# Kernel tuning notes

Hardware: AMD Instinct MI355X
Metric: run time of the kernel (lower is better)

Reference implementation:

```python
import jax, jax.numpy as jnp
import numpy as np

B, T, C = 256, 2048, 64  # batch, max_seq_len, num_classes


def setup_inputs() -> dict:
    key = jax.random.key(0)
    k1, k2, k3, k4 = jax.random.split(key, 4)
    pad_x = jax.random.normal(k1, (B, T, C), dtype=jnp.float32)
    transitions = jax.random.uniform(k2, (C, C), dtype=jnp.float32)
    origination = jax.random.uniform(k3, (C,), dtype=jnp.float32)
    batch_sizes = jnp.sort(jax.random.randint(k4, (B,), 1, T + 1))
    # the torch implementation assumes features are zero-padded past the length
    mask = jnp.arange(T)[None, :] < batch_sizes[:, None]  # (B, T)
    pad_x = pad_x * mask[:, :, None]
    return {"pad_x": pad_x, "transitions": transitions,
            "origination": origination, "batch_sizes": batch_sizes}


def reference(pad_x, transitions, origination, batch_sizes):
    # Linear-chain CRF forward algorithm (faithful to torch _forward_algo,
    # including the final sum over classes rather than logsumexp).
    x_tbc = jnp.swapaxes(pad_x, 0, 1)  # (T, B, C)
    alpha0 = x_tbc[0] + origination[None, :]  # (B, C)

    def step(alpha_prev, x_t):
        # scores[b, j, k] = alpha_prev[b, k] + transitions[j, k]
        scores = alpha_prev[:, None, :] + transitions[None, :, :]  # (B, C, C)
        alpha = x_t + jax.nn.logsumexp(scores, axis=2)  # (B, C)
        return alpha, alpha

    _, alphas_rest = jax.lax.scan(step, alpha0, x_tbc[1:])
    alphas = jnp.concatenate([alpha0[None], alphas_rest], axis=0)  # (T, B, C)
    # gather alpha at the last valid timestep of each sequence
    final = alphas[batch_sizes - 1, jnp.arange(pad_x.shape[0])]  # (B, C)
    return final.sum(axis=1)  # (B,)
```

## Files before the change

### kernel.cpp

```cpp
#include <hip/hip_runtime.h>


#define CC 64

typedef short bf16x8 __attribute__((ext_vector_type(8)));
typedef float f32x4 __attribute__((ext_vector_type(4)));

union PackAB { int w[4]; bf16x8 v; };

__device__ __forceinline__ int cvtpk(float lo, float hi) {
    int r;
    asm("v_cvt_pk_bf16_f32 %0, %1, %2" : "=v"(r) : "v"(lo), "v"(hi));
    return r;
}
__device__ __forceinline__ float bcast0(float v) {
    return __int_as_float(__builtin_amdgcn_readfirstlane(__float_as_int(v)));
}

#define LDS_FENCE() asm volatile("s_waitcnt lgkmcnt(0)" ::: "memory")

__launch_bounds__(64, 2)
__global__ void crf_seg_kernel(const float* __restrict__ x,
                               const float* __restrict__ trans,
                               const int*   __restrict__ lens,
                               unsigned short* __restrict__ Mws,
                               float* __restrict__ Ls,
                               int T, int Pseg, int Pshift, int SEG) {
    const int blk = blockIdx.x;
    const int b = blk >> Pshift;
    const int s = blk & (Pseg - 1);
    const int L = lens[b];
    const int tbeg = s * SEG;
    int segend = (s + 1) * SEG; if (segend > L - 1) segend = L - 1;
    const int nsteps = segend - tbeg;
    if (nsteps <= 0) return;

    const int l = threadIdx.x;
    const int c = l & 15, g = l >> 4;
    const float L2E = 1.4426950408889634f;
    const float* xb = x + (size_t)b * T * CC;

    __shared__ float xl[32][CC];

    {
        const int rl = l >> 4;
        const int cl = (l & 15) * 4;
        f32x4 st[8];
        #pragma unroll
        for (int i = 0; i < 8; ++i) {
            int tr = tbeg + 1 + 4 * i + rl;
            if (tr > segend) tr = segend;
            st[i] = *(const f32x4*)(xb + (size_t)tr * CC + cl);
        }
        #pragma unroll
        for (int i = 0; i < 8; ++i)
            *(f32x4*)&xl[4 * i + rl][cl] = st[i];
        LDS_FENCE();
    }

    bf16x8 A[4][2];
    #pragma unroll
    for (int mt = 0; mt < 4; ++mt) {
        const float* tr = trans + (16 * mt + c) * CC;
        #pragma unroll
        for (int ch = 0; ch < 2; ++ch) {
            float4 u = *(const float4*)(tr + 32 * ch + 4 * g);
            float4 v = *(const float4*)(tr + 32 * ch + 16 + 4 * g);
            PackAB pk;
            pk.w[0] = cvtpk(__builtin_amdgcn_exp2f(u.x * L2E), __builtin_amdgcn_exp2f(u.y * L2E));
            pk.w[1] = cvtpk(__builtin_amdgcn_exp2f(u.z * L2E), __builtin_amdgcn_exp2f(u.w * L2E));
            pk.w[2] = cvtpk(__builtin_amdgcn_exp2f(v.x * L2E), __builtin_amdgcn_exp2f(v.y * L2E));
            pk.w[3] = cvtpk(__builtin_amdgcn_exp2f(v.z * L2E), __builtin_amdgcn_exp2f(v.w * L2E));
            A[mt][ch] = pk.v;
        }
    }
    PackAB Bf[2][4];
    #pragma unroll
    for (int ch = 0; ch < 2; ++ch)
        #pragma unroll
        for (int nt = 0; nt < 4; ++nt)
            #pragma unroll
            for (int qq = 0; qq < 4; ++qq) {
                int i0 = 2 * qq, i1 = 2 * qq + 1;
                int k0 = 32 * ch + 4 * g + (i0 & 3) + 16 * (i0 >> 2);
                int k1 = 32 * ch + 4 * g + (i1 & 3) + 16 * (i1 >> 2);
                Bf[ch][nt].w[qq] = cvtpk((k0 == 16 * nt + c) ? 1.f : 0.f,
                                         (k1 == 16 * nt + c) ? 1.f : 0.f);
            }

    float Lseg = 0.f, prevS0 = 1.0f;

    for (int idx = 0; idx < nsteps; ++idx) {
        float r_   = __builtin_amdgcn_rcpf(prevS0);
        float lgr_ = __builtin_amdgcn_logf(r_);
        Lseg -= lgr_;

        const f32x4* xr = (const f32x4*)&xl[idx][0];
        f32x4 exr[4];
        #pragma unroll
        for (int mt = 0; mt < 4; ++mt) {
            f32x4 xv = xr[4 * mt + g];
            #pragma unroll
            for (int r = 0; r < 4; ++r)
                exr[mt][r] = __builtin_amdgcn_exp2f(fmaf(xv[r], L2E, lgr_));
        }

        float ns0 = 0.f;
        #pragma unroll
        for (int nt = 0; nt < 4; ++nt) {
            f32x4 Z = {0.f, 0.f, 0.f, 0.f};
            f32x4 t0, d0, d1, d2, d3;
            t0 = __builtin_amdgcn_mfma_f32_16x16x32_bf16(A[0][0], Bf[0][nt].v, Z, 0, 0, 0);
            d0 = __builtin_amdgcn_mfma_f32_16x16x32_bf16(A[0][1], Bf[1][nt].v, t0, 0, 0, 0);
            t0 = __builtin_amdgcn_mfma_f32_16x16x32_bf16(A[1][0], Bf[0][nt].v, Z, 0, 0, 0);
            d1 = __builtin_amdgcn_mfma_f32_16x16x32_bf16(A[1][1], Bf[1][nt].v, t0, 0, 0, 0);
            t0 = __builtin_amdgcn_mfma_f32_16x16x32_bf16(A[2][0], Bf[0][nt].v, Z, 0, 0, 0);
            d2 = __builtin_amdgcn_mfma_f32_16x16x32_bf16(A[2][1], Bf[1][nt].v, t0, 0, 0, 0);
            t0 = __builtin_amdgcn_mfma_f32_16x16x32_bf16(A[3][0], Bf[0][nt].v, Z, 0, 0, 0);
            d3 = __builtin_amdgcn_mfma_f32_16x16x32_bf16(A[3][1], Bf[1][nt].v, t0, 0, 0, 0);
            if (nt == 0) ns0 = d0[0];
            d0 *= exr[0]; d1 *= exr[1]; d2 *= exr[2]; d3 *= exr[3];
            Bf[0][nt].w[0] = cvtpk(d0[0], d0[1]);
            Bf[0][nt].w[1] = cvtpk(d0[2], d0[3]);
            Bf[0][nt].w[2] = cvtpk(d1[0], d1[1]);
            Bf[0][nt].w[3] = cvtpk(d1[2], d1[3]);
            Bf[1][nt].w[0] = cvtpk(d2[0], d2[1]);
            Bf[1][nt].w[1] = cvtpk(d2[2], d2[3]);
            Bf[1][nt].w[2] = cvtpk(d3[0], d3[1]);
            Bf[1][nt].w[3] = cvtpk(d3[2], d3[3]);
        }
        prevS0 = bcast0(ns0);
    }

    unsigned short* Mo = Mws + (size_t)blk * 4096;
    #pragma unroll
    for (int ch = 0; ch < 2; ++ch)
        #pragma unroll
        for (int nt = 0; nt < 4; ++nt)
            #pragma unroll
            for (int e = 0; e < 8; ++e) {
                unsigned wb = (unsigned)Bf[ch][nt].w[e >> 1];
                unsigned short hb = (e & 1) ? (unsigned short)(wb >> 16)
                                            : (unsigned short)(wb & 0xffffu);
                int row = 32 * ch + 4 * g + (e & 3) + 16 * (e >> 2);
                Mo[row * 64 + 16 * nt + c] = hb;
            }
    if (l == 0) Ls[blk] = Lseg;
}

__launch_bounds__(64, 1)
__global__ void crf_apply_kernel(const float* __restrict__ x,
                                 const float* __restrict__ orig,
                                 const int*   __restrict__ lens,
                                 const unsigned short* __restrict__ Mws,
                                 const float* __restrict__ Ls,
                                 float* __restrict__ out,
                                 int T, int Pseg, int SEG) {
    const int b = blockIdx.x, j = threadIdx.x;
    __shared__ float qb[CC];
    const float L2E = 1.4426950408889634f, LN2 = 0.6931471805599453f;
    const int L = lens[b];
    const float* xb = x + (size_t)b * T * CC;

    float Mbar = (xb[0] + orig[0]) * L2E;
    float q = __builtin_amdgcn_exp2f((xb[j] + orig[j]) * L2E - Mbar);

    uint4 R[8];
    {
        const uint4* Ms = (const uint4*)(Mws + ((size_t)b * Pseg + 0) * 4096 + j * 64);
        #pragma unroll
        for (int i = 0; i < 8; ++i) R[i] = Ms[i];
    }

    for (int s = 0; s < Pseg; ++s) {
        int tbeg = s * SEG;
        int segend = (s + 1) * SEG; if (segend > L - 1) segend = L - 1;
        if (segend - tbeg <= 0) break;

        uint4 Rc[8];
        #pragma unroll
        for (int i = 0; i < 8; ++i) Rc[i] = R[i];
        {
            int s2 = (s + 1 < Pseg) ? s + 1 : s;
            const uint4* Ms = (const uint4*)(Mws + ((size_t)b * Pseg + s2) * 4096 + j * 64);
            #pragma unroll
            for (int i = 0; i < 8; ++i) R[i] = Ms[i];
        }

        qb[j] = q;
        LDS_FENCE();

        float acc = 0.f;
        #pragma unroll
        for (int i = 0; i < 8; ++i) {
            f32x4 qv0 = *(const f32x4*)&qb[8 * i];
            f32x4 qv1 = *(const f32x4*)&qb[8 * i + 4];
            unsigned u0 = Rc[i].x, u1 = Rc[i].y, u2 = Rc[i].z, u3 = Rc[i].w;
            acc = fmaf(__uint_as_float(u0 << 16),        qv0[0], acc);
            acc = fmaf(__uint_as_float(u0 & 0xffff0000), qv0[1], acc);
            acc = fmaf(__uint_as_float(u1 << 16),        qv0[2], acc);
            acc = fmaf(__uint_as_float(u1 & 0xffff0000), qv0[3], acc);
            acc = fmaf(__uint_as_float(u2 << 16),        qv1[0], acc);
            acc = fmaf(__uint_as_float(u2 & 0xffff0000), qv1[1], acc);
            acc = fmaf(__uint_as_float(u3 << 16),        qv1[2], acc);
            acc = fmaf(__uint_as_float(u3 & 0xffff0000), qv1[3], acc);
        }
        float S = acc;
        Mbar += Ls[(size_t)b * Pseg + s];
        float p = bcast0(S);
        float r = __builtin_amdgcn_rcpf(p);
        float lgr = __builtin_amdgcn_logf(r);
        q = S * r;
        Mbar -= lgr;
        LDS_FENCE();
    }

    float alpha = LN2 * (Mbar + __builtin_amdgcn_logf(q));
    alpha += __shfl_xor(alpha, 1, 64);
    alpha += __shfl_xor(alpha, 2, 64);
    alpha += __shfl_xor(alpha, 4, 64);
    alpha += __shfl_xor(alpha, 8, 64);
    alpha += __shfl_xor(alpha, 16, 64);
    alpha += __shfl_xor(alpha, 32, 64);
    if (j == 0) out[b] = alpha;
}

extern "C" void kernel_launch(void* const* d_in, const int* in_sizes, int n_in,
                              void* d_out, int out_size, void* d_ws, size_t ws_size,
                              hipStream_t stream) {
    const float* x     = (const float*)d_in[0];
    const float* trans = (const float*)d_in[1];
    const float* orig  = (const float*)d_in[2];
    const int*   lens  = (const int*)d_in[3];
    float* out = (float*)d_out;

    const int B = in_sizes[3];
    const int T = in_sizes[0] / (B * CC);

    int P = 64, Pshift = 6;
    while (P > 1 && ws_size < (size_t)B * P * (4096 * 2 + 4)) { P >>= 1; --Pshift; }
    const int SEG = (T + P - 1) / P;

    unsigned short* Mws = (unsigned short*)d_ws;
    float* Ls = (float*)(Mws + (size_t)B * P * 4096);

    crf_seg_kernel<<<B * P, 64, 0, stream>>>(x, trans, lens, Mws, Ls, T, P, Pshift, SEG);
    crf_apply_kernel<<<B, 64, 0, stream>>>(x, orig, lens, Mws, Ls, out, T, P, SEG);
}
```

Measured before the change: 207.3 us.

## Interleave two independent segment chains per wavefront in CRF segment kernel

Each wavefront now processes two adjacent time segments, alternating steps of two independent MFMA dependency chains so one chain's matrix-core latency can hide the other's. The grid is halved and launch bounds drop to one wave per SIMD hint, since register pressure doubles with two B-fragment sets. The risk is lower occupancy and load imbalance when the second segment is short or empty.

```diff
diff --git a/kernel.cpp b/kernel.cpp
--- a/kernel.cpp
+++ b/kernel.cpp
@@ -19,7 +19,67 @@
 
 #define LDS_FENCE() asm volatile("s_waitcnt lgkmcnt(0)" ::: "memory")
 
-__launch_bounds__(64, 2)
+__device__ __forceinline__ void chain_step(const bf16x8 (&A)[4][2], PackAB (&Bf)[2][4],
+                                           const f32x4* __restrict__ xr, int g,
+                                           float& prevS0, float& Lseg) {
+    const float L2E = 1.4426950408889634f;
+    float r_   = __builtin_amdgcn_rcpf(prevS0);
+    float lgr_ = __builtin_amdgcn_logf(r_);
+    Lseg -= lgr_;
+
+    f32x4 exr[4];
+    #pragma unroll
+    for (int mt = 0; mt < 4; ++mt) {
+        f32x4 xv = xr[4 * mt + g];
+        #pragma unroll
+        for (int r = 0; r < 4; ++r)
+            exr[mt][r] = __builtin_amdgcn_exp2f(fmaf(xv[r], L2E, lgr_));
+    }
+
+    float ns0 = 0.f;
+    #pragma unroll
+    for (int nt = 0; nt < 4; ++nt) {
+        f32x4 Z = {0.f, 0.f, 0.f, 0.f};
+        f32x4 t0, d0, d1, d2, d3;
+        t0 = __builtin_amdgcn_mfma_f32_16x16x32_bf16(A[0][0], Bf[0][nt].v, Z, 0, 0, 0);
+        d0 = __builtin_amdgcn_mfma_f32_16x16x32_bf16(A[0][1], Bf[1][nt].v, t0, 0, 0, 0);
+        t0 = __builtin_amdgcn_mfma_f32_16x16x32_bf16(A[1][0], Bf[0][nt].v, Z, 0, 0, 0);
+        d1 = __builtin_amdgcn_mfma_f32_16x16x32_bf16(A[1][1], Bf[1][nt].v, t0, 0, 0, 0);
+        t0 = __builtin_amdgcn_mfma_f32_16x16x32_bf16(A[2][0], Bf[0][nt].v, Z, 0, 0, 0);
+        d2 = __builtin_amdgcn_mfma_f32_16x16x32_bf16(A[2][1], Bf[1][nt].v, t0, 0, 0, 0);
+        t0 = __builtin_amdgcn_mfma_f32_16x16x32_bf16(A[3][0], Bf[0][nt].v, Z, 0, 0, 0);
+        d3 = __builtin_amdgcn_mfma_f32_16x16x32_bf16(A[3][1], Bf[1][nt].v, t0, 0, 0, 0);
+        if (nt == 0) ns0 = d0[0];
+        d0 *= exr[0]; d1 *= exr[1]; d2 *= exr[2]; d3 *= exr[3];
+        Bf[0][nt].w[0] = cvtpk(d0[0], d0[1]);
+        Bf[0][nt].w[1] = cvtpk(d0[2], d0[3]);
+        Bf[0][nt].w[2] = cvtpk(d1[0], d1[1]);
+        Bf[0][nt].w[3] = cvtpk(d1[2], d1[3]);
+        Bf[1][nt].w[0] = cvtpk(d2[0], d2[1]);
+        Bf[1][nt].w[1] = cvtpk(d2[2], d2[3]);
+        Bf[1][nt].w[2] = cvtpk(d3[0], d3[1]);
+        Bf[1][nt].w[3] = cvtpk(d3[2], d3[3]);
+    }
+    prevS0 = bcast0(ns0);
+}
+
+__device__ __forceinline__ void store_M(unsigned short* __restrict__ Mo,
+                                        const PackAB (&Bf)[2][4], int c, int g) {
+    #pragma unroll
+    for (int ch = 0; ch < 2; ++ch)
+        #pragma unroll
+        for (int nt = 0; nt < 4; ++nt)
+            #pragma unroll
+            for (int e = 0; e < 8; ++e) {
+                unsigned wb = (unsigned)Bf[ch][nt].w[e >> 1];
+                unsigned short hb = (e & 1) ? (unsigned short)(wb >> 16)
+                                            : (unsigned short)(wb & 0xffffu);
+                int row = 32 * ch + 4 * g + (e & 3) + 16 * (e >> 2);
+                Mo[row * 64 + 16 * nt + c] = hb;
+            }
+}
+
+__launch_bounds__(64, 1)
 __global__ void crf_seg_kernel(const float* __restrict__ x,
                                const float* __restrict__ trans,
                                const int*   __restrict__ lens,
@@ -27,34 +87,52 @@
                                float* __restrict__ Ls,
                                int T, int Pseg, int Pshift, int SEG) {
     const int blk = blockIdx.x;
-    const int b = blk >> Pshift;
-    const int s = blk & (Pseg - 1);
-    const int L = lens[b];
-    const int tbeg = s * SEG;
-    int segend = (s + 1) * SEG; if (segend > L - 1) segend = L - 1;
-    const int nsteps = segend - tbeg;
-    if (nsteps <= 0) return;
+    const int b  = blk >> (Pshift - 1);
+    const int s0 = (blk & ((Pseg >> 1) - 1)) << 1;
+    const int L  = lens[b];
+
+    const int tbeg0 = s0 * SEG;
+    int se0 = (s0 + 1) * SEG; if (se0 > L - 1) se0 = L - 1;
+    const int n0 = se0 - tbeg0;
+    if (n0 <= 0) return;
+
+    const int tbeg1 = (s0 + 1) * SEG;
+    int se1 = (s0 + 2) * SEG; if (se1 > L - 1) se1 = L - 1;
+    int n1 = se1 - tbeg1; if (n1 < 0) n1 = 0;
 
     const int l = threadIdx.x;
     const int c = l & 15, g = l >> 4;
     const float L2E = 1.4426950408889634f;
     const float* xb = x + (size_t)b * T * CC;
 
-    __shared__ float xl[32][CC];
+    __shared__ float xl[2][32][CC];
 
     {
         const int rl = l >> 4;
         const int cl = (l & 15) * 4;
-        f32x4 st[8];
+        f32x4 st0[8], st1[8];
         #pragma unroll
         for (int i = 0; i < 8; ++i) {
-            int tr = tbeg + 1 + 4 * i + rl;
-            if (tr > segend) tr = segend;
-            st[i] = *(const f32x4*)(xb + (size_t)tr * CC + cl);
+            int tr = tbeg0 + 1 + 4 * i + rl;
+            if (tr > se0) tr = se0;
+            st0[i] = *(const f32x4*)(xb + (size_t)tr * CC + cl);
+        }
+        if (n1 > 0) {
+            #pragma unroll
+            for (int i = 0; i < 8; ++i) {
+                int tr = tbeg1 + 1 + 4 * i + rl;
+                if (tr > se1) tr = se1;
+                st1[i] = *(const f32x4*)(xb + (size_t)tr * CC + cl);
+            }
         }
         #pragma unroll
         for (int i = 0; i < 8; ++i)
-            *(f32x4*)&xl[4 * i + rl][cl] = st[i];
+            *(f32x4*)&xl[0][4 * i + rl][cl] = st0[i];
+        if (n1 > 0) {
+            #pragma unroll
+            for (int i = 0; i < 8; ++i)
+                *(f32x4*)&xl[1][4 * i + rl][cl] = st1[i];
+        }
         LDS_FENCE();
     }
 
@@ -74,7 +152,7 @@
             A[mt][ch] = pk.v;
         }
     }
-    PackAB Bf[2][4];
+    PackAB Bf0[2][4], Bf1[2][4];
     #pragma unroll
     for (int ch = 0; ch < 2; ++ch)
         #pragma unroll
@@ -84,68 +162,28 @@
                 int i0 = 2 * qq, i1 = 2 * qq + 1;
                 int k0 = 32 * ch + 4 * g + (i0 & 3) + 16 * (i0 >> 2);
                 int k1 = 32 * ch + 4 * g + (i1 & 3) + 16 * (i1 >> 2);
-                Bf[ch][nt].w[qq] = cvtpk((k0 == 16 * nt + c) ? 1.f : 0.f,
-                                         (k1 == 16 * nt + c) ? 1.f : 0.f);
+                int idv = cvtpk((k0 == 16 * nt + c) ? 1.f : 0.f,
+                                (k1 == 16 * nt + c) ? 1.f : 0.f);
+                Bf0[ch][nt].w[qq] = idv;
+                Bf1[ch][nt].w[qq] = idv;
             }
 
-    float Lseg = 0.f, prevS0 = 1.0f;
-
-    for (int idx = 0; idx < nsteps; ++idx) {
-        float r_   = __builtin_amdgcn_rcpf(prevS0);
-        float lgr_ = __builtin_amdgcn_logf(r_);
-        Lseg -= lgr_;
-
-        const f32x4* xr = (const f32x4*)&xl[idx][0];
-        f32x4 exr[4];
-        #pragma unroll
-        for (int mt = 0; mt < 4; ++mt) {
-            f32x4 xv = xr[4 * mt + g];
-            #pragma unroll
-            for (int r = 0; r < 4; ++r)
-                exr[mt][r] = __builtin_amdgcn_exp2f(fmaf(xv[r], L2E, lgr_));
-        }
-
-        float ns0 = 0.f;
-        #pragma unroll
-        for (int nt = 0; nt < 4; ++nt) {
-            f32x4 Z = {0.f, 0.f, 0.f, 0.f};
-            f32x4 t0, d0, d1, d2, d3;
-            t0 = __builtin_amdgcn_mfma_f32_16x16x32_bf16(A[0][0], Bf[0][nt].v, Z, 0, 0, 0);
-            d0 = __builtin_amdgcn_mfma_f32_16x16x32_bf16(A[0][1], Bf[1][nt].v, t0, 0, 0, 0);
-            t0 = __builtin_amdgcn_mfma_f32_16x16x32_bf16(A[1][0], Bf[0][nt].v, Z, 0, 0, 0);
-            d1 = __builtin_amdgcn_mfma_f32_16x16x32_bf16(A[1][1], Bf[1][nt].v, t0, 0, 0, 0);
-            t0 = __builtin_amdgcn_mfma_f32_16x16x32_bf16(A[2][0], Bf[0][nt].v, Z, 0, 0, 0);
-            d2 = __builtin_amdgcn_mfma_f32_16x16x32_bf16(A[2][1], Bf[1][nt].v, t0, 0, 0, 0);
-            t0 = __builtin_amdgcn_mfma_f32_16x16x32_bf16(A[3][0], Bf[0][nt].v, Z, 0, 0, 0);
-            d3 = __builtin_amdgcn_mfma_f32_16x16x32_bf16(A[3][1], Bf[1][nt].v, t0, 0, 0, 0);
-            if (nt == 0) ns0 = d0[0];
-            d0 *= exr[0]; d1 *= exr[1]; d2 *= exr[2]; d3 *= exr[3];
-            Bf[0][nt].w[0] = cvtpk(d0[0], d0[1]);
-            Bf[0][nt].w[1] = cvtpk(d0[2], d0[3]);
-            Bf[0][nt].w[2] = cvtpk(d1[0], d1[1]);
-            Bf[0][nt].w[3] = cvtpk(d1[2], d1[3]);
-            Bf[1][nt].w[0] = cvtpk(d2[0], d2[1]);
-            Bf[1][nt].w[1] = cvtpk(d2[2], d2[3]);
-            Bf[1][nt].w[2] = cvtpk(d3[0], d3[1]);
-            Bf[1][nt].w[3] = cvtpk(d3[2], d3[3]);
-        }
-        prevS0 = bcast0(ns0);
-    }
-
-    unsigned short* Mo = Mws + (size_t)blk * 4096;
-    #pragma unroll
-    for (int ch = 0; ch < 2; ++ch)
-        #pragma unroll
-        for (int nt = 0; nt < 4; ++nt)
-            #pragma unroll
-            for (int e = 0; e < 8; ++e) {
-                unsigned wb = (unsigned)Bf[ch][nt].w[e >> 1];
-                unsigned short hb = (e & 1) ? (unsigned short)(wb >> 16)
-                                            : (unsigned short)(wb & 0xffffu);
-                int row = 32 * ch + 4 * g + (e & 3) + 16 * (e >> 2);
-                Mo[row * 64 + 16 * nt + c] = hb;
-            }
-    if (l == 0) Ls[blk] = Lseg;
+    float Ls0 = 0.f, ps0 = 1.0f;
+    float Ls1 = 0.f, ps1 = 1.0f;
+
+    for (int idx = 0; idx < n1; ++idx) {
+        chain_step(A, Bf0, (const f32x4*)&xl[0][idx][0], g, ps0, Ls0);
+        chain_step(A, Bf1, (const f32x4*)&xl[1][idx][0], g, ps1, Ls1);
+    }
+    for (int idx = n1; idx < n0; ++idx)
+        chain_step(A, Bf0, (const f32x4*)&xl[0][idx][0], g, ps0, Ls0);
+
+    store_M(Mws + ((size_t)b * Pseg + s0) * 4096, Bf0, c, g);
+    if (l == 0) Ls[(size_t)b * Pseg + s0] = Ls0;
+    if (n1 > 0) {
+        store_M(Mws + ((size_t)b * Pseg + s0 + 1) * 4096, Bf1, c, g);
+        if (l == 0) Ls[(size_t)b * Pseg + s0 + 1] = Ls1;
+    }
 }
 
 __launch_bounds__(64, 1)
@@ -238,12 +276,13 @@
     const int T = in_sizes[0] / (B * CC);
 
     int P = 64, Pshift = 6;
-    while (P > 1 && ws_size < (size_t)B * P * (4096 * 2 + 4)) { P >>= 1; --Pshift; }
+    while (P > 2 && ws_size < (size_t)B * P * (4096 * 2 + 4)) { P >>= 1; --Pshift; }
     const int SEG = (T + P - 1) / P;
 
     unsigned short* Mws = (unsigned short*)d_ws;
     float* Ls = (float*)(Mws + (size_t)B * P * 4096);
 
-    crf_seg_kernel<<<B * P, 64, 0, stream>>>(x, trans, lens, Mws, Ls, T, P, Pshift, SEG);
+    crf_seg_kernel<<<B * (P >> 1), 64, 0, stream>>>(x, trans, lens, Mws, Ls,
+                                                    T, P, Pshift, SEG);
     crf_apply_kernel<<<B, 64, 0, stream>>>(x, orig, lens, Mws, Ls, out, T, P, SEG);
 }
```

Result: slower. 340.8 us (+64.4%).

## Loop segments within persistent blocks, precompute exp of x, renormalize every 4 steps

Applied to the files above, without the earlier changes.

The segment kernel now launches 16 blocks per batch row, and each block loops over several segments instead of one block per segment. The exponentials of the x rows are computed once while staging them into LDS. The rescaling by the first element (rcp/log) now runs once every four chain steps instead of every step, which removes transcendentals from the serial dependency chain. Occupancy hint raised to 4 blocks per CU. Renormalizing less often risks bf16/f32 overflow or precision drift over four unscaled steps, and the per-block looping can cause load imbalance since segments beyond the sequence length are skipped via break.

```diff
diff --git a/kernel.cpp b/kernel.cpp
--- a/kernel.cpp
+++ b/kernel.cpp
@@ -19,21 +19,53 @@
 
 #define LDS_FENCE() asm volatile("s_waitcnt lgkmcnt(0)" ::: "memory")
 
-__launch_bounds__(64, 2)
+template <bool SCALE>
+__device__ __forceinline__ void chain_step(const bf16x8 (&A)[4][2], PackAB (&Bf)[2][4],
+                                           const f32x4* __restrict__ er4, int g,
+                                           float r_, float& ns0) {
+    f32x4 er[4];
+    #pragma unroll
+    for (int mt = 0; mt < 4; ++mt) {
+        er[mt] = er4[4 * mt + g];
+        if (SCALE) er[mt] *= r_;
+    }
+    #pragma unroll
+    for (int nt = 0; nt < 4; ++nt) {
+        f32x4 Z = {0.f, 0.f, 0.f, 0.f};
+        f32x4 t0, d0, d1, d2, d3;
+        t0 = __builtin_amdgcn_mfma_f32_16x16x32_bf16(A[0][0], Bf[0][nt].v, Z, 0, 0, 0);
+        d0 = __builtin_amdgcn_mfma_f32_16x16x32_bf16(A[0][1], Bf[1][nt].v, t0, 0, 0, 0);
+        t0 = __builtin_amdgcn_mfma_f32_16x16x32_bf16(A[1][0], Bf[0][nt].v, Z, 0, 0, 0);
+        d1 = __builtin_amdgcn_mfma_f32_16x16x32_bf16(A[1][1], Bf[1][nt].v, t0, 0, 0, 0);
+        t0 = __builtin_amdgcn_mfma_f32_16x16x32_bf16(A[2][0], Bf[0][nt].v, Z, 0, 0, 0);
+        d2 = __builtin_amdgcn_mfma_f32_16x16x32_bf16(A[2][1], Bf[1][nt].v, t0, 0, 0, 0);
+        t0 = __builtin_amdgcn_mfma_f32_16x16x32_bf16(A[3][0], Bf[0][nt].v, Z, 0, 0, 0);
+        d3 = __builtin_amdgcn_mfma_f32_16x16x32_bf16(A[3][1], Bf[1][nt].v, t0, 0, 0, 0);
+        if (nt == 0) ns0 = d0[0];
+        d0 *= er[0]; d1 *= er[1]; d2 *= er[2]; d3 *= er[3];
+        Bf[0][nt].w[0] = cvtpk(d0[0], d0[1]);
+        Bf[0][nt].w[1] = cvtpk(d0[2], d0[3]);
+        Bf[0][nt].w[2] = cvtpk(d1[0], d1[1]);
+        Bf[0][nt].w[3] = cvtpk(d1[2], d1[3]);
+        Bf[1][nt].w[0] = cvtpk(d2[0], d2[1]);
+        Bf[1][nt].w[1] = cvtpk(d2[2], d2[3]);
+        Bf[1][nt].w[2] = cvtpk(d3[0], d3[1]);
+        Bf[1][nt].w[3] = cvtpk(d3[2], d3[3]);
+    }
+}
+
+__launch_bounds__(64, 4)
 __global__ void crf_seg_kernel(const float* __restrict__ x,
                                const float* __restrict__ trans,
                                const int*   __restrict__ lens,
                                unsigned short* __restrict__ Mws,
                                float* __restrict__ Ls,
-                               int T, int Pseg, int Pshift, int SEG) {
+                               int T, int Pseg, int NBshift, int SEG) {
     const int blk = blockIdx.x;
-    const int b = blk >> Pshift;
-    const int s = blk & (Pseg - 1);
+    const int b = blk >> NBshift;
+    const int j = blk & ((1 << NBshift) - 1);
+    const int NB = 1 << NBshift;
     const int L = lens[b];
-    const int tbeg = s * SEG;
-    int segend = (s + 1) * SEG; if (segend > L - 1) segend = L - 1;
-    const int nsteps = segend - tbeg;
-    if (nsteps <= 0) return;
 
     const int l = threadIdx.x;
     const int c = l & 15, g = l >> 4;
@@ -41,22 +73,6 @@
     const float* xb = x + (size_t)b * T * CC;
 
     __shared__ float xl[32][CC];
-
-    {
-        const int rl = l >> 4;
-        const int cl = (l & 15) * 4;
-        f32x4 st[8];
-        #pragma unroll
-        for (int i = 0; i < 8; ++i) {
-            int tr = tbeg + 1 + 4 * i + rl;
-            if (tr > segend) tr = segend;
-            st[i] = *(const f32x4*)(xb + (size_t)tr * CC + cl);
-        }
-        #pragma unroll
-        for (int i = 0; i < 8; ++i)
-            *(f32x4*)&xl[4 * i + rl][cl] = st[i];
-        LDS_FENCE();
-    }
 
     bf16x8 A[4][2];
     #pragma unroll
@@ -74,7 +90,7 @@
             A[mt][ch] = pk.v;
         }
     }
-    PackAB Bf[2][4];
+    PackAB Bid[2][4];
     #pragma unroll
     for (int ch = 0; ch < 2; ++ch)
         #pragma unroll
@@ -84,68 +100,73 @@
                 int i0 = 2 * qq, i1 = 2 * qq + 1;
                 int k0 = 32 * ch + 4 * g + (i0 & 3) + 16 * (i0 >> 2);
                 int k1 = 32 * ch + 4 * g + (i1 & 3) + 16 * (i1 >> 2);
-                Bf[ch][nt].w[qq] = cvtpk((k0 == 16 * nt + c) ? 1.f : 0.f,
-                                         (k1 == 16 * nt + c) ? 1.f : 0.f);
-            }
-
-    float Lseg = 0.f, prevS0 = 1.0f;
-
-    for (int idx = 0; idx < nsteps; ++idx) {
-        float r_   = __builtin_amdgcn_rcpf(prevS0);
-        float lgr_ = __builtin_amdgcn_logf(r_);
-        Lseg -= lgr_;
-
-        const f32x4* xr = (const f32x4*)&xl[idx][0];
-        f32x4 exr[4];
-        #pragma unroll
-        for (int mt = 0; mt < 4; ++mt) {
-            f32x4 xv = xr[4 * mt + g];
-            #pragma unroll
-            for (int r = 0; r < 4; ++r)
-                exr[mt][r] = __builtin_amdgcn_exp2f(fmaf(xv[r], L2E, lgr_));
-        }
-
-        float ns0 = 0.f;
-        #pragma unroll
-        for (int nt = 0; nt < 4; ++nt) {
-            f32x4 Z = {0.f, 0.f, 0.f, 0.f};
-            f32x4 t0, d0, d1, d2, d3;
-            t0 = __builtin_amdgcn_mfma_f32_16x16x32_bf16(A[0][0], Bf[0][nt].v, Z, 0, 0, 0);
-            d0 = __builtin_amdgcn_mfma_f32_16x16x32_bf16(A[0][1], Bf[1][nt].v, t0, 0, 0, 0);
-            t0 = __builtin_amdgcn_mfma_f32_16x16x32_bf16(A[1][0], Bf[0][nt].v, Z, 0, 0, 0);
-            d1 = __builtin_amdgcn_mfma_f32_16x16x32_bf16(A[1][1], Bf[1][nt].v, t0, 0, 0, 0);
-            t0 = __builtin_amdgcn_mfma_f32_16x16x32_bf16(A[2][0], Bf[0][nt].v, Z, 0, 0, 0);
-            d2 = __builtin_amdgcn_mfma_f32_16x16x32_bf16(A[2][1], Bf[1][nt].v, t0, 0, 0, 0);
-            t0 = __builtin_amdgcn_mfma_f32_16x16x32_bf16(A[3][0], Bf[0][nt].v, Z, 0, 0, 0);
-            d3 = __builtin_amdgcn_mfma_f32_16x16x32_bf16(A[3][1], Bf[1][nt].v, t0, 0, 0, 0);
-            if (nt == 0) ns0 = d0[0];
-            d0 *= exr[0]; d1 *= exr[1]; d2 *= exr[2]; d3 *= exr[3];
-            Bf[0][nt].w[0] = cvtpk(d0[0], d0[1]);
-            Bf[0][nt].w[1] = cvtpk(d0[2], d0[3]);
-            Bf[0][nt].w[2] = cvtpk(d1[0], d1[1]);
-            Bf[0][nt].w[3] = cvtpk(d1[2], d1[3]);
-            Bf[1][nt].w[0] = cvtpk(d2[0], d2[1]);
-            Bf[1][nt].w[1] = cvtpk(d2[2], d2[3]);
-            Bf[1][nt].w[2] = cvtpk(d3[0], d3[1]);
-            Bf[1][nt].w[3] = cvtpk(d3[2], d3[3]);
-        }
-        prevS0 = bcast0(ns0);
-    }
-
-    unsigned short* Mo = Mws + (size_t)blk * 4096;
-    #pragma unroll
-    for (int ch = 0; ch < 2; ++ch)
-        #pragma unroll
-        for (int nt = 0; nt < 4; ++nt)
-            #pragma unroll
-            for (int e = 0; e < 8; ++e) {
-                unsigned wb = (unsigned)Bf[ch][nt].w[e >> 1];
-                unsigned short hb = (e & 1) ? (unsigned short)(wb >> 16)
-                                            : (unsigned short)(wb & 0xffffu);
-                int row = 32 * ch + 4 * g + (e & 3) + 16 * (e >> 2);
-                Mo[row * 64 + 16 * nt + c] = hb;
-            }
-    if (l == 0) Ls[blk] = Lseg;
+                Bid[ch][nt].w[qq] = cvtpk((k0 == 16 * nt + c) ? 1.f : 0.f,
+                                          (k1 == 16 * nt + c) ? 1.f : 0.f);
+            }
+
+    for (int s = j; s < Pseg; s += NB) {
+        const int tbeg = s * SEG;
+        int segend = (s + 1) * SEG; if (segend > L - 1) segend = L - 1;
+        const int nsteps = segend - tbeg;
+        if (nsteps <= 0) break;
+
+        {
+            const int rl = l >> 4;
+            const int cl = (l & 15) * 4;
+            LDS_FENCE();
+            f32x4 st[8];
+            #pragma unroll
+            for (int i = 0; i < 8; ++i) {
+                int tr = tbeg + 1 + 4 * i + rl;
+                if (tr > segend) tr = segend;
+                st[i] = *(const f32x4*)(xb + (size_t)tr * CC + cl);
+            }
+            #pragma unroll
+            for (int i = 0; i < 8; ++i) {
+                f32x4 e;
+                #pragma unroll
+                for (int r = 0; r < 4; ++r)
+                    e[r] = __builtin_amdgcn_exp2f(st[i][r] * L2E);
+                *(f32x4*)&xl[4 * i + rl][cl] = e;
+            }
+            LDS_FENCE();
+        }
+
+        PackAB Bf[2][4];
+        #pragma unroll
+        for (int ch = 0; ch < 2; ++ch)
+            #pragma unroll
+            for (int nt = 0; nt < 4; ++nt) Bf[ch][nt] = Bid[ch][nt];
+
+        float Lseg = 0.f, ns0 = 1.0f;
+        for (int base = 0; base < nsteps; base += 4) {
+            float r_ = 1.0f;
+            if (base > 0) {
+                float S00 = bcast0(ns0);
+                r_ = __builtin_amdgcn_rcpf(S00);
+                Lseg -= __builtin_amdgcn_logf(r_);
+            }
+            chain_step<true >(A, Bf, (const f32x4*)&xl[base][0], g, r_, ns0);
+            if (base + 1 < nsteps) chain_step<false>(A, Bf, (const f32x4*)&xl[base + 1][0], g, 1.f, ns0);
+            if (base + 2 < nsteps) chain_step<false>(A, Bf, (const f32x4*)&xl[base + 2][0], g, 1.f, ns0);
+            if (base + 3 < nsteps) chain_step<false>(A, Bf, (const f32x4*)&xl[base + 3][0], g, 1.f, ns0);
+        }
+
+        unsigned short* Mo = Mws + ((size_t)b * Pseg + s) * 4096;
+        #pragma unroll
+        for (int ch = 0; ch < 2; ++ch)
+            #pragma unroll
+            for (int nt = 0; nt < 4; ++nt)
+                #pragma unroll
+                for (int e = 0; e < 8; ++e) {
+                    unsigned wb = (unsigned)Bf[ch][nt].w[e >> 1];
+                    unsigned short hb = (e & 1) ? (unsigned short)(wb >> 16)
+                                                : (unsigned short)(wb & 0xffffu);
+                    int row = 32 * ch + 4 * g + (e & 3) + 16 * (e >> 2);
+                    Mo[row * 64 + 16 * nt + c] = hb;
+                }
+        if (l == 0) Ls[(size_t)b * Pseg + s] = Lseg;
+    }
 }
 
 __launch_bounds__(64, 1)
@@ -237,13 +258,15 @@
     const int B = in_sizes[3];
     const int T = in_sizes[0] / (B * CC);
 
-    int P = 64, Pshift = 6;
-    while (P > 1 && ws_size < (size_t)B * P * (4096 * 2 + 4)) { P >>= 1; --Pshift; }
+    int P = 64;
+    while (P > 16 && ws_size < (size_t)B * P * (4096 * 2 + 4)) P >>= 1;
     const int SEG = (T + P - 1) / P;
+    const int NBshift = 4;
 
     unsigned short* Mws = (unsigned short*)d_ws;
     float* Ls = (float*)(Mws + (size_t)B * P * 4096);
 
-    crf_seg_kernel<<<B * P, 64, 0, stream>>>(x, trans, lens, Mws, Ls, T, P, Pshift, SEG);
+    crf_seg_kernel<<<B * 16, 64, 0, stream>>>(x, trans, lens, Mws, Ls,
+                                              T, P, NBshift, SEG);
     crf_apply_kernel<<<B, 64, 0, stream>>>(x, orig, lens, Mws, Ls, out, T, P, SEG);
 }
```

Result: faster. 197.5 us (-4.7%).
